# Performance work log

Hardware: AMD Instinct MI355X
Metric: run time of the kernel (lower is better)

## Reference

```python
import jax, jax.numpy as jnp
import numpy as np

B, F, H, N, S = 1024, 256, 256, 128, 2
DEV_MIN, DEV_MAX = 0.001, 0.01
LOG2PI = float(np.log(2.0 * np.pi))  # k/2*log(2pi) with k=2


def setup_inputs() -> dict:
    key = jax.random.key(0)
    ks = jax.random.split(key, 16)
    d = {}
    d['latents'] = jax.random.normal(ks[0], (B, F), jnp.float32)
    d['realPoints'] = jax.random.uniform(ks[1], (B, 2), jnp.float32)
    d['predMu'] = jax.random.uniform(ks[2], (B, 2), jnp.float32)
    d['predScale'] = 0.01 + 0.05 * jax.random.uniform(ks[3], (B, 2), jnp.float32)
    d['eps'] = jax.random.normal(ks[4], (S, B * N, 2), jnp.float32)
    dims = [F] + [H] * 5
    for i in range(5):
        d[f'W{i}'] = jax.random.normal(ks[5 + i], (dims[i], dims[i + 1]), jnp.float32) / np.sqrt(dims[i])
        d[f'b{i}'] = jnp.zeros((dims[i + 1],), jnp.float32)
    d['Wp'] = jax.random.normal(ks[10], (N, H, 2), jnp.float32) / np.sqrt(H)
    d['bp'] = jnp.zeros((N, 2), jnp.float32)
    return d


def _mvn_logprob(x, mu, s):
    # diagonal 2D Gaussian log_prob; broadcasts over leading dims
    z = (x - mu) / s
    return -0.5 * jnp.sum(z * z, axis=-1) - jnp.sum(jnp.log(s), axis=-1) - LOG2PI


def reference(latents, realPoints, predMu, predScale, eps,
              W0, b0, W1, b1, W2, b2, W3, b3, W4, b4, Wp, bp):
    h = latents
    for W, b in ((W0, b0), (W1, b1), (W2, b2), (W3, b3), (W4, b4)):
        h = jax.nn.relu(h @ W + b)
    mu = 0.5 + jnp.einsum('bh,nhk->bnk', h, Wp) + bp          # (B, N, 2)
    Bn, Nn = mu.shape[0], mu.shape[1]
    dev = jnp.linspace(DEV_MIN, DEV_MAX, Nn)[:, None]          # (N, 1)
    scale = jnp.tile(dev, (Bn, 2))                             # (B*N, 2)
    muF = mu.reshape(Bn * Nn, 2)

    # real-points loss: log_prob of each real point under all N gaussians, sigmoid
    pts_real = jnp.repeat(realPoints, Nn, axis=0)              # (B*N, 2)
    realLoss = jax.nn.sigmoid(_mvn_logprob(pts_real, muF, scale).reshape(Bn, Nn))

    # reparameterized samples: (S, B*N, 2) -> (S*N, B, 2)
    sampled = muF + scale * eps
    sampled = sampled.reshape(S, Bn, Nn, 2).transpose(0, 2, 1, 3).reshape(S * Nn, Bn, 2)

    # discriminator lossA: log_prob under detached predicted dist, sigmoid(-x), MSLE vs 0.5
    pmD = jax.lax.stop_gradient(predMu)
    psD = jax.lax.stop_gradient(predScale)
    la = _mvn_logprob(sampled, pmD, psD)                       # (S*N, B)
    la = la.reshape(S, Nn, Bn).transpose(2, 1, 0)              # (B, N, S)
    la = jax.nn.sigmoid(-la)
    lossA = jnp.mean(jnp.square(jnp.log1p(0.5) - jnp.log1p(la)), axis=-1)  # (B, N)

    # discriminator lossB: all-pairs log_prob of samples under own gaussians
    # equivalent to tf.repeat(sampled, N, axis=-2) then log_prob against (B*N,) batch
    z = (sampled[:, :, None, :] - mu[None, :, :, :]) / dev     # (S*N, B, N, 2)
    lb = -0.5 * jnp.sum(z * z, axis=-1) - 2.0 * jnp.log(dev[:, 0]) - LOG2PI  # (S*N, B, N)
    lb = lb.reshape(S, Nn, Bn, Nn).transpose(2, 1, 0, 3)       # (B, N, S, N)
    sm = jax.nn.softmax(lb, axis=-1)
    idx = jnp.arange(Nn)[None, :, None, None]
    diag = jnp.take_along_axis(sm, idx, axis=-1)[..., 0]       # (B, N, S)
    lossB = jnp.square(1.0 - diag)

    # generator loss: log_prob of detached samples under (non-detached) predicted dist
    gl = _mvn_logprob(jax.lax.stop_gradient(sampled), predMu, predScale)  # (S*N, B)
    gl = jax.nn.sigmoid(gl).reshape(S, Nn, Bn).transpose(2, 1, 0)
    gl = jnp.mean(gl, axis=-1)                                 # (B, N)
    genLoss = gl * jax.lax.stop_gradient(1.0 - realLoss)

    return (sampled, genLoss, realLoss, lossA, lossB)
```

## Files before the change

### kernel.cpp

```cpp
#include <hip/hip_runtime.h>
#include <math.h>

#define BB   1024
#define HH   256
#define NN   128
#define SS   2
#define RR   4
#define LOG2PI_F 1.8378770664093453f
#define DEV_MIN_F 0.001f
#define DEV_STEP_F 7.08661417322835e-05f
#define LOG1P_HALF 0.40546510810816438f
#define SHIFT_F 12.0f

#define OFF_GEN  524288
#define OFF_REAL 655360
#define OFF_A    786432
#define OFF_B    917504

#define GLD2(dst, ptr, OFS) \
    asm volatile("global_load_dwordx2 %0, %1, off offset:" OFS \
                 : "=v"(dst) : "v"(ptr))

#define LOADBANK(S, P)                                            \
    {                                                             \
        const float* _pp = (P);                                   \
        GLD2(S[0], _pp, "-4096"); GLD2(S[1], _pp, "-3072");       \
        GLD2(S[2], _pp, "-2048"); GLD2(S[3], _pp, "-1024");       \
        GLD2(S[4], _pp, "0");     GLD2(S[5], _pp, "1024");        \
        GLD2(S[6], _pp, "2048");  GLD2(S[7], _pp, "3072");        \
    }

#define GATEN(S, CNT)                                                      \
    asm volatile("s_waitcnt vmcnt(" CNT ")"                                \
                 : "+v"(S[0]), "+v"(S[1]), "+v"(S[2]), "+v"(S[3]),         \
                   "+v"(S[4]), "+v"(S[5]), "+v"(S[6]), "+v"(S[7]))

#define BAR_LDS()                                                 \
    {                                                             \
        asm volatile("s_waitcnt lgkmcnt(0)" ::: "memory");        \
        __builtin_amdgcn_s_barrier();                             \
        asm volatile("" ::: "memory");                            \
    }

__global__ __launch_bounds__(256) void transpose_wp_kernel(
    const float* __restrict__ Wp, float* __restrict__ Wt) {
    const int k = blockIdx.x;
    const int j = threadIdx.x;
    Wt[k * 256 + j] = Wp[(j >> 1) * 512 + k * 2 + (j & 1)];
}

__global__ __launch_bounds__(1024, 4) void mlp_loss_kernel(
    const float* __restrict__ latents, const float* __restrict__ eps,
    const float* __restrict__ realPts, const float* __restrict__ predMu,
    const float* __restrict__ predScale,
    const float* __restrict__ W0, const float* __restrict__ b0,
    const float* __restrict__ W1, const float* __restrict__ b1,
    const float* __restrict__ W2, const float* __restrict__ b2,
    const float* __restrict__ W3, const float* __restrict__ b3,
    const float* __restrict__ W4, const float* __restrict__ b4,
    const float* __restrict__ Wt, const float* __restrict__ bp,
    float* __restrict__ out) {
    __shared__ float  hbuf[2][RR][256];
    __shared__ float  part[8][RR][256];
    __shared__ float  sbias[6][256];
    __shared__ float2 sprm[NN];

    const int t  = threadIdx.x;
    const int q  = t >> 7;
    const int c  = t & 127;
    const int rL = t >> 8;
    const int j  = t & 255;
    const int brow = blockIdx.x * RR;

    if (t < NN) {
        float dv = DEV_MIN_F + (float)t * DEV_STEP_F;
        sprm[t] = make_float2(-0.5f / (dv * dv), -2.f * __logf(dv) - LOG2PI_F);
    }
    hbuf[0][rL][j] = latents[(brow + rL) * 256 + j];
    #pragma unroll
    for (int ii = 0; ii < 2; ++ii) {
        int idx = t + ii * 1024;
        if (idx < 1536) {
            int Lb = idx >> 8, jj = idx & 255;
            const float* bsrc = (Lb == 0) ? b0 : (Lb == 1) ? b1 : (Lb == 2) ? b2
                              : (Lb == 3) ? b3 : (Lb == 4) ? b4 : bp;
            sbias[Lb][jj] = bsrc[jj];
        }
    }
    const int nL = j >> 1, sL = j & 1;
    const int b = brow + rL;
    const float2 epv = ((const float2*)eps)[sL * (BB * NN) + b * NN + nL];
    const float2 pm  = ((const float2*)predMu)[b];
    const float2 ps  = ((const float2*)predScale)[b];
    const float2 rp  = ((const float2*)realPts)[b];

    BAR_LDS();

    const float* Wsrc[6] = {W0, W1, W2, W3, W4, Wt};
    const int coff = 2 * c + 1024;

    float2 bk[3][8];
    LOADBANK(bk[0], W0 + (q * 32 + 0) * 256 + coff);
    LOADBANK(bk[1], W0 + (q * 32 + 8) * 256 + coff);

    #pragma unroll
    for (int L = 0; L < 6; ++L) {
        const int cur = L & 1;
        float2 acc0 = {0.f, 0.f}, acc1 = {0.f, 0.f};
        float2 acc2 = {0.f, 0.f}, acc3 = {0.f, 0.f};
        #pragma unroll
        for (int i = 0; i < 4; ++i) {
            const int gb = L * 4 + i;
            const int nb = gb + 2;
            if (nb < 24) {
                LOADBANK(bk[nb % 3],
                         Wsrc[nb >> 2] + (q * 32 + (nb & 3) * 8) * 256 + coff);
            }
            if (gb <= 21)      { GATEN(bk[gb % 3], "16"); }
            else if (gb == 22) { GATEN(bk[gb % 3], "8");  }
            else               { GATEN(bk[gb % 3], "0");  }
            const int kb = q * 32 + i * 8;
            float4 hA0 = *(const float4*)&hbuf[cur][0][kb];
            float4 hB0 = *(const float4*)&hbuf[cur][0][kb + 4];
            float4 hA1 = *(const float4*)&hbuf[cur][1][kb];
            float4 hB1 = *(const float4*)&hbuf[cur][1][kb + 4];
            float4 hA2 = *(const float4*)&hbuf[cur][2][kb];
            float4 hB2 = *(const float4*)&hbuf[cur][2][kb + 4];
            float4 hA3 = *(const float4*)&hbuf[cur][3][kb];
            float4 hB3 = *(const float4*)&hbuf[cur][3][kb + 4];
            const float2* S = bk[gb % 3];
            #pragma unroll
            for (int kk = 0; kk < 8; ++kk) {
                float2 wv = S[kk];
                float h0 = (kk < 4) ? (&hA0.x)[kk] : (&hB0.x)[kk - 4];
                float h1 = (kk < 4) ? (&hA1.x)[kk] : (&hB1.x)[kk - 4];
                float h2 = (kk < 4) ? (&hA2.x)[kk] : (&hB2.x)[kk - 4];
                float h3 = (kk < 4) ? (&hA3.x)[kk] : (&hB3.x)[kk - 4];
                acc0.x = fmaf(h0, wv.x, acc0.x); acc0.y = fmaf(h0, wv.y, acc0.y);
                acc1.x = fmaf(h1, wv.x, acc1.x); acc1.y = fmaf(h1, wv.y, acc1.y);
                acc2.x = fmaf(h2, wv.x, acc2.x); acc2.y = fmaf(h2, wv.y, acc2.y);
                acc3.x = fmaf(h3, wv.x, acc3.x); acc3.y = fmaf(h3, wv.y, acc3.y);
            }
        }
        ((float2*)&part[q][0][0])[c] = acc0;
        ((float2*)&part[q][1][0])[c] = acc1;
        ((float2*)&part[q][2][0])[c] = acc2;
        ((float2*)&part[q][3][0])[c] = acc3;
        BAR_LDS();
        float val = 0.f;
        #pragma unroll
        for (int p = 0; p < 8; ++p) val += part[p][rL][j];
        val += sbias[L][j];
        if (L == 5) val += 0.5f;
        else        val = fmaxf(val, 0.f);
        hbuf[cur ^ 1][rL][j] = val;
        BAR_LDS();
    }

    const float* __restrict__ muL = &hbuf[0][rL][0];
    const int n = nL, s = sL;
    const float devn = DEV_MIN_F + (float)n * DEV_STEP_F;
    const float2 prn = sprm[n];

    const float mux = muL[2 * n], muy = muL[2 * n + 1];
    const float px = fmaf(devn, epv.x, mux);
    const float py = fmaf(devn, epv.y, muy);

    ((float2*)out)[(size_t)(s * NN + n) * BB + b] = make_float2(px, py);

    float sum0 = 0.f, sum1 = 0.f;
    #pragma unroll 4
    for (int m = 0; m < NN; m += 2) {
        float4 mm = *(const float4*)&muL[2 * m];
        float4 pr = *(const float4*)&sprm[m];
        float dx0 = px - mm.x, dy0 = py - mm.y;
        float lb0 = fmaf(fmaf(dx0, dx0, dy0 * dy0), pr.x, pr.y);
        sum0 += __expf(lb0 - SHIFT_F);
        float dx1 = px - mm.z, dy1 = py - mm.w;
        float lb1 = fmaf(fmaf(dx1, dx1, dy1 * dy1), pr.z, pr.w);
        sum1 += __expf(lb1 - SHIFT_F);
    }
    float dxd = devn * epv.x, dyd = devn * epv.y;
    float lbd = fmaf(fmaf(dxd, dxd, dyd * dyd), prn.x, prn.y);
    float ed  = __expf(lbd - SHIFT_F);
    float diag = ed / (sum0 + sum1);
    float lbv = (1.f - diag) * (1.f - diag);
    out[OFF_B + (size_t)b * (NN * SS) + j] = lbv;

    float zx = (px - pm.x) / ps.x, zy = (py - pm.y) / ps.y;
    float la = -0.5f * (zx * zx + zy * zy) - __logf(ps.x) - __logf(ps.y) - LOG2PI_F;
    float aa = 1.f / (1.f + __expf(la));
    float termA = LOG1P_HALF - log1pf(aa);
    termA = termA * termA;
    float gg = 1.f / (1.f + __expf(-la));

    float drx = rp.x - mux, dry = rp.y - muy;
    float lr = fmaf(fmaf(drx, drx, dry * dry), prn.x, prn.y);
    float rl = 1.f / (1.f + __expf(-lr));

    float termA_sum = termA + __shfl_xor(termA, 1);
    float gg_sum    = gg + __shfl_xor(gg, 1);
    if (s == 0) {
        out[OFF_GEN  + (size_t)b * NN + n] = 0.5f * gg_sum * (1.f - rl);
        out[OFF_REAL + (size_t)b * NN + n] = rl;
        out[OFF_A    + (size_t)b * NN + n] = 0.5f * termA_sum;
    }
}

extern "C" void kernel_launch(void* const* d_in, const int* in_sizes, int n_in,
                              void* d_out, int out_size, void* d_ws, size_t ws_size,
                              hipStream_t stream) {
    const float* latents   = (const float*)d_in[0];
    const float* realPts   = (const float*)d_in[1];
    const float* predMu    = (const float*)d_in[2];
    const float* predScale = (const float*)d_in[3];
    const float* eps       = (const float*)d_in[4];
    const float* W0 = (const float*)d_in[5];
    const float* b0 = (const float*)d_in[6];
    const float* W1 = (const float*)d_in[7];
    const float* b1 = (const float*)d_in[8];
    const float* W2 = (const float*)d_in[9];
    const float* b2 = (const float*)d_in[10];
    const float* W3 = (const float*)d_in[11];
    const float* b3 = (const float*)d_in[12];
    const float* W4 = (const float*)d_in[13];
    const float* b4 = (const float*)d_in[14];
    const float* Wp = (const float*)d_in[15];
    const float* bp = (const float*)d_in[16];

    float* Wtp = (float*)d_ws;

    transpose_wp_kernel<<<dim3(256), dim3(256), 0, stream>>>(Wp, Wtp);
    mlp_loss_kernel<<<dim3(BB / RR), dim3(1024), 0, stream>>>(
        latents, eps, realPts, predMu, predScale,
        W0, b0, W1, b1, W2, b2, W3, b3, W4, b4, Wtp, bp, (float*)d_out);
}
```

Baseline: 125.5 us.

## Remap MLP GEMV to 16 k-groups with float4 weights; split pairwise softmax across lanes

The hand-scheduled inline-asm triple-buffered weight prefetch is replaced by plain float4 loads. Each thread now covers 4 output columns over 16 k-rows, and partial sums are reduced in two stages: the upper half of the groups adds into the lower half in LDS before the 8-way sum. Biases move from LDS into registers and the h ping-pong buffer becomes a single buffer. In the all-pairs lossB loop, each lane in a quad handles a quarter of the m range for all four quad points, with shuffle reductions, to cut redundant LDS reads. The cost is losing explicit load/compute overlap and adding an extra barrier per layer.

Result: faster. 120.5 us (-4.0%).

```diff
diff --git a/kernel.cpp b/kernel.cpp
--- a/kernel.cpp
+++ b/kernel.cpp
@@ -17,29 +17,14 @@
 #define OFF_A    786432
 #define OFF_B    917504
 
-#define GLD2(dst, ptr, OFS) \
-    asm volatile("global_load_dwordx2 %0, %1, off offset:" OFS \
-                 : "=v"(dst) : "v"(ptr))
-
-#define LOADBANK(S, P)                                            \
+typedef float f4_t __attribute__((ext_vector_type(4)));
+
+#define FMA4(ACC, HS, WV)                                         \
     {                                                             \
-        const float* _pp = (P);                                   \
-        GLD2(S[0], _pp, "-4096"); GLD2(S[1], _pp, "-3072");       \
-        GLD2(S[2], _pp, "-2048"); GLD2(S[3], _pp, "-1024");       \
-        GLD2(S[4], _pp, "0");     GLD2(S[5], _pp, "1024");        \
-        GLD2(S[6], _pp, "2048");  GLD2(S[7], _pp, "3072");        \
-    }
-
-#define GATEN(S, CNT)                                                      \
-    asm volatile("s_waitcnt vmcnt(" CNT ")"                                \
-                 : "+v"(S[0]), "+v"(S[1]), "+v"(S[2]), "+v"(S[3]),         \
-                   "+v"(S[4]), "+v"(S[5]), "+v"(S[6]), "+v"(S[7]))
-
-#define BAR_LDS()                                                 \
-    {                                                             \
-        asm volatile("s_waitcnt lgkmcnt(0)" ::: "memory");        \
-        __builtin_amdgcn_s_barrier();                             \
-        asm volatile("" ::: "memory");                            \
+        ACC.x = fmaf(HS, WV.x, ACC.x);                            \
+        ACC.y = fmaf(HS, WV.y, ACC.y);                            \
+        ACC.z = fmaf(HS, WV.z, ACC.z);                            \
+        ACC.w = fmaf(HS, WV.w, ACC.w);                            \
     }
 
 __global__ __launch_bounds__(256) void transpose_wp_kernel(
@@ -60,14 +45,13 @@
     const float* __restrict__ W4, const float* __restrict__ b4,
     const float* __restrict__ Wt, const float* __restrict__ bp,
     float* __restrict__ out) {
-    __shared__ float  hbuf[2][RR][256];
-    __shared__ float  part[8][RR][256];
-    __shared__ float  sbias[6][256];
+    __shared__ __align__(16) float hb[RR][256];
+    __shared__ __align__(16) float part[8][RR][256];
     __shared__ float2 sprm[NN];
 
     const int t  = threadIdx.x;
-    const int q  = t >> 7;
-    const int c  = t & 127;
+    const int q  = t >> 6;
+    const int c  = t & 63;
     const int rL = t >> 8;
     const int j  = t & 255;
     const int brow = blockIdx.x * RR;
@@ -76,88 +60,71 @@
         float dv = DEV_MIN_F + (float)t * DEV_STEP_F;
         sprm[t] = make_float2(-0.5f / (dv * dv), -2.f * __logf(dv) - LOG2PI_F);
     }
-    hbuf[0][rL][j] = latents[(brow + rL) * 256 + j];
-    #pragma unroll
-    for (int ii = 0; ii < 2; ++ii) {
-        int idx = t + ii * 1024;
-        if (idx < 1536) {
-            int Lb = idx >> 8, jj = idx & 255;
-            const float* bsrc = (Lb == 0) ? b0 : (Lb == 1) ? b1 : (Lb == 2) ? b2
-                              : (Lb == 3) ? b3 : (Lb == 4) ? b4 : bp;
-            sbias[Lb][jj] = bsrc[jj];
-        }
-    }
+    hb[rL][j] = latents[(brow + rL) * 256 + j];
+
+    float biasv[6];
+    biasv[0] = b0[j]; biasv[1] = b1[j]; biasv[2] = b2[j];
+    biasv[3] = b3[j]; biasv[4] = b4[j]; biasv[5] = bp[j];
+
     const int nL = j >> 1, sL = j & 1;
     const int b = brow + rL;
     const float2 epv = ((const float2*)eps)[sL * (BB * NN) + b * NN + nL];
-    const float2 pm  = ((const float2*)predMu)[b];
-    const float2 ps  = ((const float2*)predScale)[b];
-    const float2 rp  = ((const float2*)realPts)[b];
-
-    BAR_LDS();
+
+    __syncthreads();
 
     const float* Wsrc[6] = {W0, W1, W2, W3, W4, Wt};
-    const int coff = 2 * c + 1024;
-
-    float2 bk[3][8];
-    LOADBANK(bk[0], W0 + (q * 32 + 0) * 256 + coff);
-    LOADBANK(bk[1], W0 + (q * 32 + 8) * 256 + coff);
 
     #pragma unroll
     for (int L = 0; L < 6; ++L) {
-        const int cur = L & 1;
-        float2 acc0 = {0.f, 0.f}, acc1 = {0.f, 0.f};
-        float2 acc2 = {0.f, 0.f}, acc3 = {0.f, 0.f};
+        const float* __restrict__ Wb = Wsrc[L] + (q * 16) * 256 + 4 * c;
+        f4_t acc[4];
+        #pragma unroll
+        for (int r = 0; r < 4; ++r) acc[r] = (f4_t)0.f;
+
         #pragma unroll
         for (int i = 0; i < 4; ++i) {
-            const int gb = L * 4 + i;
-            const int nb = gb + 2;
-            if (nb < 24) {
-                LOADBANK(bk[nb % 3],
-                         Wsrc[nb >> 2] + (q * 32 + (nb & 3) * 8) * 256 + coff);
-            }
-            if (gb <= 21)      { GATEN(bk[gb % 3], "16"); }
-            else if (gb == 22) { GATEN(bk[gb % 3], "8");  }
-            else               { GATEN(bk[gb % 3], "0");  }
-            const int kb = q * 32 + i * 8;
-            float4 hA0 = *(const float4*)&hbuf[cur][0][kb];
-            float4 hB0 = *(const float4*)&hbuf[cur][0][kb + 4];
-            float4 hA1 = *(const float4*)&hbuf[cur][1][kb];
-            float4 hB1 = *(const float4*)&hbuf[cur][1][kb + 4];
-            float4 hA2 = *(const float4*)&hbuf[cur][2][kb];
-            float4 hB2 = *(const float4*)&hbuf[cur][2][kb + 4];
-            float4 hA3 = *(const float4*)&hbuf[cur][3][kb];
-            float4 hB3 = *(const float4*)&hbuf[cur][3][kb + 4];
-            const float2* S = bk[gb % 3];
+            f4_t w0 = *(const f4_t*)(Wb + (i * 4 + 0) * 256);
+            f4_t w1 = *(const f4_t*)(Wb + (i * 4 + 1) * 256);
+            f4_t w2 = *(const f4_t*)(Wb + (i * 4 + 2) * 256);
+            f4_t w3 = *(const f4_t*)(Wb + (i * 4 + 3) * 256);
+            const int kb = q * 16 + i * 4;
             #pragma unroll
-            for (int kk = 0; kk < 8; ++kk) {
-                float2 wv = S[kk];
-                float h0 = (kk < 4) ? (&hA0.x)[kk] : (&hB0.x)[kk - 4];
-                float h1 = (kk < 4) ? (&hA1.x)[kk] : (&hB1.x)[kk - 4];
-                float h2 = (kk < 4) ? (&hA2.x)[kk] : (&hB2.x)[kk - 4];
-                float h3 = (kk < 4) ? (&hA3.x)[kk] : (&hB3.x)[kk - 4];
-                acc0.x = fmaf(h0, wv.x, acc0.x); acc0.y = fmaf(h0, wv.y, acc0.y);
-                acc1.x = fmaf(h1, wv.x, acc1.x); acc1.y = fmaf(h1, wv.y, acc1.y);
-                acc2.x = fmaf(h2, wv.x, acc2.x); acc2.y = fmaf(h2, wv.y, acc2.y);
-                acc3.x = fmaf(h3, wv.x, acc3.x); acc3.y = fmaf(h3, wv.y, acc3.y);
+            for (int r = 0; r < 4; ++r) {
+                f4_t hv = *(const f4_t*)&hb[r][kb];
+                FMA4(acc[r], hv.x, w0);
+                FMA4(acc[r], hv.y, w1);
+                FMA4(acc[r], hv.z, w2);
+                FMA4(acc[r], hv.w, w3);
             }
         }
-        ((float2*)&part[q][0][0])[c] = acc0;
-        ((float2*)&part[q][1][0])[c] = acc1;
-        ((float2*)&part[q][2][0])[c] = acc2;
-        ((float2*)&part[q][3][0])[c] = acc3;
-        BAR_LDS();
-        float val = 0.f;
-        #pragma unroll
-        for (int p = 0; p < 8; ++p) val += part[p][rL][j];
-        val += sbias[L][j];
+
+        if (q < 8) {
+            #pragma unroll
+            for (int r = 0; r < 4; ++r)
+                *(f4_t*)&part[q][r][4 * c] = acc[r];
+        }
+        __syncthreads();
+        if (q >= 8) {
+            #pragma unroll
+            for (int r = 0; r < 4; ++r) {
+                f4_t tmp = *(const f4_t*)&part[q - 8][r][4 * c];
+                acc[r] += tmp;
+                *(f4_t*)&part[q - 8][r][4 * c] = acc[r];
+            }
+        }
+        __syncthreads();
+
+        float val = part[0][rL][j] + part[1][rL][j] + part[2][rL][j] +
+                    part[3][rL][j] + part[4][rL][j] + part[5][rL][j] +
+                    part[6][rL][j] + part[7][rL][j];
+        val += biasv[L];
         if (L == 5) val += 0.5f;
         else        val = fmaxf(val, 0.f);
-        hbuf[cur ^ 1][rL][j] = val;
-        BAR_LDS();
-    }
-
-    const float* __restrict__ muL = &hbuf[0][rL][0];
+        hb[rL][j] = val;
+        __syncthreads();
+    }
+
+    const float* __restrict__ muL = &hb[rL][0];
     const int n = nL, s = sL;
     const float devn = DEV_MIN_F + (float)n * DEV_STEP_F;
     const float2 prn = sprm[n];
@@ -168,22 +135,56 @@
 
     ((float2*)out)[(size_t)(s * NN + n) * BB + b] = make_float2(px, py);
 
-    float sum0 = 0.f, sum1 = 0.f;
+    const float2 pm = ((const float2*)predMu)[b];
+    const float2 ps = ((const float2*)predScale)[b];
+    const float2 rp = ((const float2*)realPts)[b];
+
+    const int me = t & 3;
+    float x1 = __shfl_xor(px, 1), y1 = __shfl_xor(py, 1);
+    float x2 = __shfl_xor(px, 2), y2 = __shfl_xor(py, 2);
+    float x3 = __shfl_xor(px, 3), y3 = __shfl_xor(py, 3);
+    float PX0 = (me == 0) ? px : (me == 1) ? x1 : (me == 2) ? x2 : x3;
+    float PY0 = (me == 0) ? py : (me == 1) ? y1 : (me == 2) ? y2 : y3;
+    float PX1 = (me == 1) ? px : (me == 0) ? x1 : (me == 3) ? x2 : x3;
+    float PY1 = (me == 1) ? py : (me == 0) ? y1 : (me == 3) ? y2 : y3;
+    float PX2 = (me == 2) ? px : (me == 3) ? x1 : (me == 0) ? x2 : x3;
+    float PY2 = (me == 2) ? py : (me == 3) ? y1 : (me == 0) ? y2 : y3;
+    float PX3 = (me == 3) ? px : (me == 2) ? x1 : (me == 1) ? x2 : x3;
+    float PY3 = (me == 3) ? py : (me == 2) ? y1 : (me == 1) ? y2 : y3;
+
+    float S0 = 0.f, S1 = 0.f, S2 = 0.f, S3 = 0.f;
     #pragma unroll 4
-    for (int m = 0; m < NN; m += 2) {
-        float4 mm = *(const float4*)&muL[2 * m];
-        float4 pr = *(const float4*)&sprm[m];
-        float dx0 = px - mm.x, dy0 = py - mm.y;
-        float lb0 = fmaf(fmaf(dx0, dx0, dy0 * dy0), pr.x, pr.y);
-        sum0 += __expf(lb0 - SHIFT_F);
-        float dx1 = px - mm.z, dy1 = py - mm.w;
-        float lb1 = fmaf(fmaf(dx1, dx1, dy1 * dy1), pr.z, pr.w);
-        sum1 += __expf(lb1 - SHIFT_F);
-    }
+    for (int mi = 0; mi < 16; ++mi) {
+        f4_t mm = *(const f4_t*)&muL[16 * mi + 4 * me];
+        f4_t pr = *(const f4_t*)((const float*)sprm + 16 * mi + 4 * me);
+        float dx, dy, lb;
+        dx = PX0 - mm.x; dy = PY0 - mm.y;
+        lb = fmaf(fmaf(dx, dx, dy * dy), pr.x, pr.y); S0 += __expf(lb - SHIFT_F);
+        dx = PX1 - mm.x; dy = PY1 - mm.y;
+        lb = fmaf(fmaf(dx, dx, dy * dy), pr.x, pr.y); S1 += __expf(lb - SHIFT_F);
+        dx = PX2 - mm.x; dy = PY2 - mm.y;
+        lb = fmaf(fmaf(dx, dx, dy * dy), pr.x, pr.y); S2 += __expf(lb - SHIFT_F);
+        dx = PX3 - mm.x; dy = PY3 - mm.y;
+        lb = fmaf(fmaf(dx, dx, dy * dy), pr.x, pr.y); S3 += __expf(lb - SHIFT_F);
+        dx = PX0 - mm.z; dy = PY0 - mm.w;
+        lb = fmaf(fmaf(dx, dx, dy * dy), pr.z, pr.w); S0 += __expf(lb - SHIFT_F);
+        dx = PX1 - mm.z; dy = PY1 - mm.w;
+        lb = fmaf(fmaf(dx, dx, dy * dy), pr.z, pr.w); S1 += __expf(lb - SHIFT_F);
+        dx = PX2 - mm.z; dy = PY2 - mm.w;
+        lb = fmaf(fmaf(dx, dx, dy * dy), pr.z, pr.w); S2 += __expf(lb - SHIFT_F);
+        dx = PX3 - mm.z; dy = PY3 - mm.w;
+        lb = fmaf(fmaf(dx, dx, dy * dy), pr.z, pr.w); S3 += __expf(lb - SHIFT_F);
+    }
+    S0 += __shfl_xor(S0, 1); S1 += __shfl_xor(S1, 1);
+    S2 += __shfl_xor(S2, 1); S3 += __shfl_xor(S3, 1);
+    S0 += __shfl_xor(S0, 2); S1 += __shfl_xor(S1, 2);
+    S2 += __shfl_xor(S2, 2); S3 += __shfl_xor(S3, 2);
+    float sum = (me == 0) ? S0 : (me == 1) ? S1 : (me == 2) ? S2 : S3;
+
     float dxd = devn * epv.x, dyd = devn * epv.y;
     float lbd = fmaf(fmaf(dxd, dxd, dyd * dyd), prn.x, prn.y);
     float ed  = __expf(lbd - SHIFT_F);
-    float diag = ed / (sum0 + sum1);
+    float diag = ed / sum;
     float lbv = (1.f - diag) * (1.f - diag);
     out[OFF_B + (size_t)b * (NN * SS) + j] = lbv;
 
```
